# Kernel tuning notes

Hardware: AMD Instinct MI355X
Metric: run time of the kernel (lower is better)

Reference implementation:

```python
import jax, jax.numpy as jnp
import numpy as np

B, T, D, H = 2, 2048, 1024, 16
DK = D // H


def setup_inputs() -> dict:
    key = jax.random.key(0)
    ks = jax.random.split(key, 11)
    s = 1.0 / np.sqrt(D)
    return {
        "x_q": jax.random.normal(ks[0], (B, T, D), jnp.float32),
        "x_kv": jax.random.normal(ks[1], (B, T, D), jnp.float32),
        "mask": jnp.ones((B, 1, T, T), jnp.int32),
        "Wq": jax.random.normal(ks[2], (D, D), jnp.float32) * s,
        "bq": jnp.zeros((D,), jnp.float32),
        "Wk": jax.random.normal(ks[3], (D, D), jnp.float32) * s,
        "bk": jnp.zeros((D,), jnp.float32),
        "Wv": jax.random.normal(ks[4], (D, D), jnp.float32) * s,
        "bv": jnp.zeros((D,), jnp.float32),
        "Wo": jax.random.normal(ks[5], (D, D), jnp.float32) * s,
        "bo": jnp.zeros((D,), jnp.float32),
    }


def _split_heads(x):
    # (B, T, D) -> (B, H, T, DK)
    b, t, _ = x.shape
    return x.reshape(b, t, H, DK).transpose(0, 2, 1, 3)


def reference(x_q, x_kv, mask, Wq, bq, Wk, bk, Wv, bv, Wo, bo):
    # Linear layers use torch convention: y = x @ W.T + b
    Q = _split_heads(x_q @ Wq.T + bq)   # (B,H,Tq,DK)
    K = _split_heads(x_kv @ Wk.T + bk)  # (B,H,Tk,DK)
    V = _split_heads(x_kv @ Wv.T + bv)  # (B,H,Tk,DK)

    scores = jnp.einsum("bhqd,bhkd->bhqk", Q, K) / jnp.sqrt(jnp.float32(DK))
    scores = jnp.where(mask == 0, jnp.float32(-jnp.inf), scores)
    attn = jax.nn.softmax(scores, axis=-1)  # (B,H,Tq,Tk)

    out = jnp.einsum("bhqk,bhkd->bhqd", attn, V)
    out = out.transpose(0, 2, 1, 3).reshape(B, T, D)  # combine heads
    out = out @ Wo.T + bo
    return out, attn
```

## Files before the change

kernel.cpp:

```cpp
#include <hip/hip_runtime.h>
#include <hip/hip_bf16.h>

#define DEVINL __device__ __forceinline__

typedef __attribute__((ext_vector_type(4))) float f32x4;
typedef __attribute__((ext_vector_type(8))) short short8;

constexpr int CB = 2, CT = 2048, CD = 1024, CH = 16, CDK = 64;
constexpr int CM = CB * CT;
constexpr float LOG2E = 1.44269504088896340736f;

DEVINL ushort f2bf(float f) {
  __hip_bfloat16 h = __float2bfloat16(f);
  ushort u; __builtin_memcpy(&u, &h, 2); return u;
}

DEVINL void gl2lds16(const ushort* g, ushort* ldsbase) {
  __builtin_amdgcn_global_load_lds(
      (const __attribute__((address_space(1))) void*)g,
      (__attribute__((address_space(3))) void*)ldsbase, 16, 0, 0);
}

__global__ void cvt_all_kernel(const float* __restrict__ s0, ushort* __restrict__ d0, int n0,
                               const float* __restrict__ s1, ushort* __restrict__ d1, int n1,
                               const float* __restrict__ s2, ushort* __restrict__ d2, int n2,
                               const float* __restrict__ s3, ushort* __restrict__ d3, int n3,
                               const float* __restrict__ s4, ushort* __restrict__ d4, int n4,
                               const float* __restrict__ s5, ushort* __restrict__ d5, int n5)
{
  int i = (blockIdx.x * blockDim.x + threadIdx.x) * 4;
  const float* s; ushort* d;
  if (i < n0) { s = s0; d = d0; }
  else if ((i -= n0) < n1) { s = s1; d = d1; }
  else if ((i -= n1) < n2) { s = s2; d = d2; }
  else if ((i -= n2) < n3) { s = s3; d = d3; }
  else if ((i -= n3) < n4) { s = s4; d = d4; }
  else if ((i -= n4) < n5) { s = s5; d = d5; }
  else return;
  float4 v = *reinterpret_cast<const float4*>(s + i);
  ushort4 o;
  o.x = f2bf(v.x); o.y = f2bf(v.y); o.z = f2bf(v.z); o.w = f2bf(v.w);
  *reinterpret_cast<ushort4*>(d + i) = o;
}

__global__ void mask_flags_kernel(const int* __restrict__ mask, uint* __restrict__ flags) {
  const int tile = blockIdx.x;
  const int b = tile >> 10, qb = (tile >> 5) & 31, kb = tile & 31;
  const int* base = mask + ((size_t)b * CT + qb * 64) * CT + kb * 64;
  const int r = threadIdx.x >> 2, c0 = (threadIdx.x & 3) * 16;
  int ok = 1;
  for (int j = 0; j < 4; ++j) {
    int4 v = *reinterpret_cast<const int4*>(base + (size_t)r * CT + c0 + j * 4);
    ok &= (v.x != 0) & (v.y != 0) & (v.z != 0) & (v.w != 0);
  }
  __shared__ int red[4];
  unsigned long long bal = __ballot(ok);
  if ((threadIdx.x & 63) == 0) red[threadIdx.x >> 6] = (bal == ~0ull);
  __syncthreads();
  if (threadIdx.x == 0) flags[tile] = (uint)(red[0] & red[1] & red[2] & red[3]);
}

__global__ __launch_bounds__(256, 2)
void gemm_nt_kernel(const ushort* __restrict__ A, const ushort* __restrict__ Bm,
                    const float* __restrict__ bias1, const float* __restrict__ bias2,
                    void* __restrict__ Out, void* __restrict__ Out2,
                    int M, int N, int K, int mode, float scale)
{
  constexpr int BM = 128, BN = 64, BK = 32;
  __shared__ __align__(16) ushort As[2][BM * BK];
  __shared__ __align__(16) ushort Bs[2][BN * BK];
  const int tid = threadIdx.x;
  const int lane = tid & 63, wid = tid >> 6;
  const int wr = wid >> 1, wc = wid & 1;
  const int bm0 = blockIdx.y * BM, bn0 = blockIdx.x * BN;
  const int rsel = lane & 15, ksel = (lane >> 4) * 8;
  const int srow = lane >> 2, sc8 = (lane & 3) * 8;

  f32x4 acc[4][2];
  for (int i = 0; i < 4; ++i) for (int j = 0; j < 2; ++j) acc[i][j] = f32x4{0.f, 0.f, 0.f, 0.f};

  auto stage = [&](int bu, int k0) {
    const int ra0 = wid * 32;
    gl2lds16(&A[(size_t)(bm0 + ra0 + srow) * K + k0 + sc8],      &As[bu][ra0 * BK]);
    gl2lds16(&A[(size_t)(bm0 + ra0 + 16 + srow) * K + k0 + sc8], &As[bu][(ra0 + 16) * BK]);
    const int rb0 = wid * 16;
    gl2lds16(&Bm[(size_t)(bn0 + rb0 + srow) * K + k0 + sc8],     &Bs[bu][rb0 * BK]);
  };

  stage(0, 0);
  __syncthreads();
  const int NKT = K / BK;
  int bu = 0;
  for (int kt = 0; kt < NKT; ++kt) {
    if (kt + 1 < NKT) stage(bu ^ 1, (kt + 1) * BK);
    short8 af[4], bfr[2];
    for (int mi = 0; mi < 4; ++mi)
      af[mi] = *reinterpret_cast<short8*>(&As[bu][(wr * 64 + mi * 16 + rsel) * BK + ksel]);
    for (int ni = 0; ni < 2; ++ni)
      bfr[ni] = *reinterpret_cast<short8*>(&Bs[bu][(wc * 32 + ni * 16 + rsel) * BK + ksel]);
    for (int mi = 0; mi < 4; ++mi)
      for (int ni = 0; ni < 2; ++ni)
        acc[mi][ni] = __builtin_amdgcn_mfma_f32_16x16x32_bf16(af[mi], bfr[ni], acc[mi][ni], 0, 0, 0);
    if (kt + 1 < NKT) { __syncthreads(); bu ^= 1; }
  }

  const int r0 = (lane >> 4) * 4;
  for (int mi = 0; mi < 4; ++mi)
    for (int ni = 0; ni < 2; ++ni) {
      int gj = bn0 + wc * 32 + ni * 16 + rsel;
      float bv = (mode == 3 && gj >= 1024) ? bias2[gj - 1024] : bias1[gj];
      for (int r = 0; r < 4; ++r) {
        int gi = bm0 + wr * 64 + mi * 16 + r0 + r;
        float v = (acc[mi][ni][r] + bv) * scale;
        if (mode == 2) {
          reinterpret_cast<float*>(Out)[(size_t)gi * N + gj] = v;
        } else {
          int bb = gi >> 11, t = gi & (CT - 1);
          if (mode == 3 && gj >= 1024) {
            int gjv = gj - 1024;
            reinterpret_cast<ushort*>(Out2)[(((size_t)(bb * CH + (gjv >> 6)) * CDK + (gjv & 63)) * CT + t)] = f2bf(v);
          } else {
            reinterpret_cast<ushort*>(Out)[(((size_t)(bb * CH + (gj >> 6)) * CT + t) * CDK + (gj & 63))] = f2bf(v);
          }
        }
      }
    }
}

__global__ __launch_bounds__(512, 2)
void attn_kernel(const ushort* __restrict__ Qb, const ushort* __restrict__ Kb,
                 const ushort* __restrict__ Vt, const int* __restrict__ mask,
                 const uint* __restrict__ flags,
                 float* __restrict__ attn_out, ushort* __restrict__ oh)
{
  constexpr int KB = 64, LDK = 72;
  __shared__ __align__(16) ushort Ks[KB * LDK];
  __shared__ __align__(16) ushort Vs[CDK * LDK];
  __shared__ __align__(16) ushort Ps[8][16 * LDK];

  const int tid = threadIdx.x, wid = tid >> 6, lane = tid & 63;
  const int bh = blockIdx.y, b = bh >> 4, h = bh & 15;
  const int q0 = blockIdx.x * 128 + wid * 16;
  const int rsel = lane & 15, grp = lane >> 4, ksel = grp * 8;
  const int srow = tid >> 3, scol = (tid & 7) * 8;
  const uint* fl = flags + (b << 10) + ((q0 >> 6) << 5);

  short8 qa0, qa1;
  {
    const ushort* qrow = Qb + ((size_t)bh * CT + q0 + rsel) * CDK;
    qa0 = *reinterpret_cast<const short8*>(qrow + ksel);
    qa1 = *reinterpret_cast<const short8*>(qrow + 32 + ksel);
  }

  float l_part[4] = {0.f, 0.f, 0.f, 0.f};
  const int* mrow = mask + (size_t)b * CT * CT;

  for (int k0 = 0; k0 < CT; k0 += KB) {
    __syncthreads();
    *reinterpret_cast<short8*>(&Ks[srow * LDK + scol]) =
        *reinterpret_cast<const short8*>(&Kb[((size_t)bh * CT + k0 + srow) * CDK + scol]);
    __syncthreads();
    const uint f = fl[k0 >> 6];
    for (int ni = 0; ni < 4; ++ni) {
      f32x4 z = {0.f, 0.f, 0.f, 0.f};
      short8 kb0 = *reinterpret_cast<short8*>(&Ks[(ni * 16 + rsel) * LDK + ksel]);
      short8 kb1 = *reinterpret_cast<short8*>(&Ks[(ni * 16 + rsel) * LDK + 32 + ksel]);
      z = __builtin_amdgcn_mfma_f32_16x16x32_bf16(qa0, kb0, z, 0, 0, 0);
      z = __builtin_amdgcn_mfma_f32_16x16x32_bf16(qa1, kb1, z, 0, 0, 0);
      if (f) {
        for (int r = 0; r < 4; ++r) l_part[r] += exp2f(z[r]);
      } else {
        int kk = k0 + ni * 16 + rsel;
        for (int r = 0; r < 4; ++r) {
          int q = q0 + grp * 4 + r;
          l_part[r] += mrow[(size_t)q * CT + kk] ? exp2f(z[r]) : 0.f;
        }
      }
    }
  }
  for (int off = 1; off < 16; off <<= 1)
    for (int r = 0; r < 4; ++r) l_part[r] += __shfl_xor(l_part[r], off, 64);
  float inv_l[4];
  for (int r = 0; r < 4; ++r) inv_l[r] = 1.f / l_part[r];

  f32x4 oacc[4];
  for (int nd = 0; nd < 4; ++nd) oacc[nd] = f32x4{0.f, 0.f, 0.f, 0.f};
  float* arow = attn_out + (size_t)bh * CT * CT;
  ushort* pw = &Ps[wid][0];

  for (int k0 = 0; k0 < CT; k0 += KB) {
    __syncthreads();
    *reinterpret_cast<short8*>(&Ks[srow * LDK + scol]) =
        *reinterpret_cast<const short8*>(&Kb[((size_t)bh * CT + k0 + srow) * CDK + scol]);
    *reinterpret_cast<short8*>(&Vs[srow * LDK + scol]) =
        *reinterpret_cast<const short8*>(&Vt[((size_t)bh * CDK + srow) * CT + k0 + scol]);
    __syncthreads();
    const uint f = fl[k0 >> 6];
    for (int ni = 0; ni < 4; ++ni) {
      f32x4 z = {0.f, 0.f, 0.f, 0.f};
      short8 kb0 = *reinterpret_cast<short8*>(&Ks[(ni * 16 + rsel) * LDK + ksel]);
      short8 kb1 = *reinterpret_cast<short8*>(&Ks[(ni * 16 + rsel) * LDK + 32 + ksel]);
      z = __builtin_amdgcn_mfma_f32_16x16x32_bf16(qa0, kb0, z, 0, 0, 0);
      z = __builtin_amdgcn_mfma_f32_16x16x32_bf16(qa1, kb1, z, 0, 0, 0);
      int kk = k0 + ni * 16 + rsel;
      for (int r = 0; r < 4; ++r) {
        int q = q0 + grp * 4 + r;
        float p;
        if (f) p = exp2f(z[r]);
        else   p = mrow[(size_t)q * CT + kk] ? exp2f(z[r]) : 0.f;
        arow[(size_t)q * CT + kk] = p * inv_l[r];
        pw[(grp * 4 + r) * LDK + ni * 16 + rsel] = f2bf(p);
      }
    }
    short8 pa0 = *reinterpret_cast<short8*>(&pw[rsel * LDK + ksel]);
    short8 pa1 = *reinterpret_cast<short8*>(&pw[rsel * LDK + 32 + ksel]);
    for (int nd = 0; nd < 4; ++nd) {
      short8 vb0 = *reinterpret_cast<short8*>(&Vs[(nd * 16 + rsel) * LDK + ksel]);
      short8 vb1 = *reinterpret_cast<short8*>(&Vs[(nd * 16 + rsel) * LDK + 32 + ksel]);
      oacc[nd] = __builtin_amdgcn_mfma_f32_16x16x32_bf16(pa0, vb0, oacc[nd], 0, 0, 0);
      oacc[nd] = __builtin_amdgcn_mfma_f32_16x16x32_bf16(pa1, vb1, oacc[nd], 0, 0, 0);
    }
  }

  for (int nd = 0; nd < 4; ++nd)
    for (int r = 0; r < 4; ++r) {
      int q = q0 + grp * 4 + r, d = nd * 16 + rsel;
      oh[((size_t)b * CT + q) * CD + h * CDK + d] = f2bf(oacc[nd][r] * inv_l[r]);
    }
}

extern "C" void kernel_launch(void* const* d_in, const int* in_sizes, int n_in,
                              void* d_out, int out_size, void* d_ws, size_t ws_size,
                              hipStream_t stream)
{
  const float* x_q  = (const float*)d_in[0];
  const float* x_kv = (const float*)d_in[1];
  const int*   mask = (const int*)d_in[2];
  const float* Wq = (const float*)d_in[3];
  const float* bq = (const float*)d_in[4];
  const float* Wk = (const float*)d_in[5];
  const float* bk = (const float*)d_in[6];
  const float* Wv = (const float*)d_in[7];
  const float* bv = (const float*)d_in[8];
  const float* Wo = (const float*)d_in[9];
  const float* bo = (const float*)d_in[10];

  float* out  = (float*)d_out;
  float* attn = out + (size_t)CB * CT * CD;

  char* w = (char*)d_ws;
  auto alloc = [&](size_t bytes) { char* p = w; w += (bytes + 255) & ~(size_t)255; return p; };
  ushort* xq_bf  = (ushort*)alloc((size_t)CM * CD * 2);
  ushort* xkv_bf = (ushort*)alloc((size_t)CM * CD * 2);
  ushort* Wq_bf  = (ushort*)alloc((size_t)CD * CD * 2);
  ushort* Wk_bf  = (ushort*)alloc((size_t)CD * CD * 2);
  ushort* Wv_bf  = (ushort*)alloc((size_t)CD * CD * 2);
  ushort* Wo_bf  = (ushort*)alloc((size_t)CD * CD * 2);
  ushort* Q_bf   = (ushort*)alloc((size_t)CM * CD * 2);
  ushort* K_bf   = (ushort*)alloc((size_t)CM * CD * 2);
  ushort* Vt_bf  = (ushort*)alloc((size_t)CM * CD * 2);
  ushort* oh_bf  = (ushort*)alloc((size_t)CM * CD * 2);
  uint*   mflags = (uint*)alloc(2048 * sizeof(uint));

  {
    const int nx = CM * CD, nw = CD * CD;
    const int total_quads = (2 * nx + 4 * nw) / 4;
    const int blocks = (total_quads + 255) / 256;
    hipLaunchKernelGGL(cvt_all_kernel, dim3(blocks), dim3(256), 0, stream,
                       x_q, xq_bf, nx, x_kv, xkv_bf, nx,
                       Wq, Wq_bf, nw, Wk, Wk_bf, nw,
                       Wv, Wv_bf, nw, Wo, Wo_bf, nw);
  }

  hipLaunchKernelGGL(mask_flags_kernel, dim3(2048), dim3(256), 0, stream, mask, mflags);

  hipLaunchKernelGGL(gemm_nt_kernel, dim3(CD / 64, CM / 128), dim3(256), 0, stream,
                     xq_bf, Wq_bf, bq, bq, (void*)Q_bf, nullptr, CM, CD, CD, 0, 0.125f * LOG2E);
  hipLaunchKernelGGL(gemm_nt_kernel, dim3(2 * CD / 64, CM / 128), dim3(256), 0, stream,
                     xkv_bf, Wk_bf, bk, bv, (void*)K_bf, (void*)Vt_bf, CM, 2 * CD, CD, 3, 1.0f);

  hipLaunchKernelGGL(attn_kernel, dim3(CT / 128, CB * CH), dim3(512), 0, stream,
                     Q_bf, K_bf, Vt_bf, mask, mflags, attn, oh_bf);

  hipLaunchKernelGGL(gemm_nt_kernel, dim3(CD / 64, CM / 128), dim3(256), 0, stream,
                     oh_bf, Wo_bf, bo, bo, d_out, nullptr, CM, CD, CD, 2, 1.0f);
}
```

Baseline: 331.5 us.

## Double-buffer K/V via async global-to-LDS loads with swizzle and transposed QK MFMA

Replaces the synchronous K/V LDS staging with double-buffered global_load_lds copies into XOR-swizzled LDS tiles, so the next tile's load overlaps compute and one barrier per iteration is removed. The QK MFMA operands are swapped so each lane holds four consecutive keys for one query row, which allows float4 stores of the attention matrix and packed 4-wide stores of P into LDS. The row-sum reduction is reorganized to match, and inverse norms are shuffled back for the output layout. This adds more LDS and relies on the swizzle matching the async copy layout.

```diff
diff --git a/kernel.cpp b/kernel.cpp
--- a/kernel.cpp
+++ b/kernel.cpp
@@ -5,6 +5,7 @@
 
 typedef __attribute__((ext_vector_type(4))) float f32x4;
 typedef __attribute__((ext_vector_type(8))) short short8;
+typedef __attribute__((ext_vector_type(4))) short short4v;
 
 constexpr int CB = 2, CT = 2048, CD = 1024, CH = 16, CDK = 64;
 constexpr int CM = CB * CT;
@@ -133,17 +134,28 @@
                  const uint* __restrict__ flags,
                  float* __restrict__ attn_out, ushort* __restrict__ oh)
 {
-  constexpr int KB = 64, LDK = 72;
-  __shared__ __align__(16) ushort Ks[KB * LDK];
-  __shared__ __align__(16) ushort Vs[CDK * LDK];
-  __shared__ __align__(16) ushort Ps[8][16 * LDK];
+  constexpr int LDP = 72;
+  __shared__ __align__(16) ushort Ks[2][64 * 64];
+  __shared__ __align__(16) ushort Vs[2][64 * 64];
+  __shared__ __align__(16) ushort Ps[8][16 * LDP];
 
   const int tid = threadIdx.x, wid = tid >> 6, lane = tid & 63;
   const int bh = blockIdx.y, b = bh >> 4, h = bh & 15;
   const int q0 = blockIdx.x * 128 + wid * 16;
   const int rsel = lane & 15, grp = lane >> 4, ksel = grp * 8;
-  const int srow = tid >> 3, scol = (tid & 7) * 8;
+  const int swz = rsel & 7;
   const uint* fl = flags + (b << 10) + ((q0 >> 6) << 5);
+  const ushort* kpan = Kb + (size_t)bh * CT * CDK;
+  const ushort* vpan = Vt + (size_t)bh * CDK * CT;
+
+  const int strow = tid >> 3, stc = (tid & 7) ^ (strow & 7);
+
+  auto stageK = [&](int bu, int k0) {
+    gl2lds16(&kpan[(size_t)(k0 + strow) * CDK + stc * 8], &Ks[bu][(size_t)wid * 512]);
+  };
+  auto stageV = [&](int bu, int k0) {
+    gl2lds16(&vpan[(size_t)strow * CT + k0 + stc * 8], &Vs[bu][(size_t)wid * 512]);
+  };
 
   short8 qa0, qa1;
   {
@@ -152,80 +164,94 @@
     qa1 = *reinterpret_cast<const short8*>(qrow + 32 + ksel);
   }
 
-  float l_part[4] = {0.f, 0.f, 0.f, 0.f};
   const int* mrow = mask + (size_t)b * CT * CT;
-
-  for (int k0 = 0; k0 < CT; k0 += KB) {
+  const int qme = q0 + rsel;
+
+  float l_lane = 0.f;
+  stageK(0, 0);
+  __syncthreads();
+  int bu = 0;
+  for (int kt = 0; kt < 32; ++kt) {
+    const int k0 = kt * 64;
+    if (kt + 1 < 32) stageK(bu ^ 1, k0 + 64);
+    const uint f = fl[kt];
+    for (int ni = 0; ni < 4; ++ni) {
+      const int krow = ni * 16 + rsel;
+      short8 kb0 = *reinterpret_cast<short8*>(&Ks[bu][krow * 64 + ((grp    ) ^ swz) * 8]);
+      short8 kb1 = *reinterpret_cast<short8*>(&Ks[bu][krow * 64 + ((grp + 4) ^ swz) * 8]);
+      f32x4 z = {0.f, 0.f, 0.f, 0.f};
+      z = __builtin_amdgcn_mfma_f32_16x16x32_bf16(kb0, qa0, z, 0, 0, 0);
+      z = __builtin_amdgcn_mfma_f32_16x16x32_bf16(kb1, qa1, z, 0, 0, 0);
+      if (f) {
+        l_lane += exp2f(z[0]) + exp2f(z[1]) + exp2f(z[2]) + exp2f(z[3]);
+      } else {
+        const int kb_ = k0 + ni * 16 + grp * 4;
+        for (int r = 0; r < 4; ++r)
+          l_lane += mrow[(size_t)qme * CT + kb_ + r] ? exp2f(z[r]) : 0.f;
+      }
+    }
     __syncthreads();
-    *reinterpret_cast<short8*>(&Ks[srow * LDK + scol]) =
-        *reinterpret_cast<const short8*>(&Kb[((size_t)bh * CT + k0 + srow) * CDK + scol]);
-    __syncthreads();
-    const uint f = fl[k0 >> 6];
-    for (int ni = 0; ni < 4; ++ni) {
-      f32x4 z = {0.f, 0.f, 0.f, 0.f};
-      short8 kb0 = *reinterpret_cast<short8*>(&Ks[(ni * 16 + rsel) * LDK + ksel]);
-      short8 kb1 = *reinterpret_cast<short8*>(&Ks[(ni * 16 + rsel) * LDK + 32 + ksel]);
-      z = __builtin_amdgcn_mfma_f32_16x16x32_bf16(qa0, kb0, z, 0, 0, 0);
-      z = __builtin_amdgcn_mfma_f32_16x16x32_bf16(qa1, kb1, z, 0, 0, 0);
-      if (f) {
-        for (int r = 0; r < 4; ++r) l_part[r] += exp2f(z[r]);
-      } else {
-        int kk = k0 + ni * 16 + rsel;
-        for (int r = 0; r < 4; ++r) {
-          int q = q0 + grp * 4 + r;
-          l_part[r] += mrow[(size_t)q * CT + kk] ? exp2f(z[r]) : 0.f;
-        }
-      }
-    }
-  }
-  for (int off = 1; off < 16; off <<= 1)
-    for (int r = 0; r < 4; ++r) l_part[r] += __shfl_xor(l_part[r], off, 64);
-  float inv_l[4];
-  for (int r = 0; r < 4; ++r) inv_l[r] = 1.f / l_part[r];
+    bu ^= 1;
+  }
+  l_lane += __shfl_xor(l_lane, 16, 64);
+  l_lane += __shfl_xor(l_lane, 32, 64);
+  const float inv_l = 1.f / l_lane;
 
   f32x4 oacc[4];
   for (int nd = 0; nd < 4; ++nd) oacc[nd] = f32x4{0.f, 0.f, 0.f, 0.f};
-  float* arow = attn_out + (size_t)bh * CT * CT;
+  float* aq = attn_out + (size_t)bh * CT * CT + (size_t)qme * CT;
   ushort* pw = &Ps[wid][0];
 
-  for (int k0 = 0; k0 < CT; k0 += KB) {
-    __syncthreads();
-    *reinterpret_cast<short8*>(&Ks[srow * LDK + scol]) =
-        *reinterpret_cast<const short8*>(&Kb[((size_t)bh * CT + k0 + srow) * CDK + scol]);
-    *reinterpret_cast<short8*>(&Vs[srow * LDK + scol]) =
-        *reinterpret_cast<const short8*>(&Vt[((size_t)bh * CDK + srow) * CT + k0 + scol]);
-    __syncthreads();
-    const uint f = fl[k0 >> 6];
+  stageK(0, 0);
+  stageV(0, 0);
+  __syncthreads();
+  bu = 0;
+  for (int kt = 0; kt < 32; ++kt) {
+    const int k0 = kt * 64;
+    if (kt + 1 < 32) { stageK(bu ^ 1, k0 + 64); stageV(bu ^ 1, k0 + 64); }
+    const uint f = fl[kt];
     for (int ni = 0; ni < 4; ++ni) {
+      const int krow = ni * 16 + rsel;
+      short8 kb0 = *reinterpret_cast<short8*>(&Ks[bu][krow * 64 + ((grp    ) ^ swz) * 8]);
+      short8 kb1 = *reinterpret_cast<short8*>(&Ks[bu][krow * 64 + ((grp + 4) ^ swz) * 8]);
       f32x4 z = {0.f, 0.f, 0.f, 0.f};
-      short8 kb0 = *reinterpret_cast<short8*>(&Ks[(ni * 16 + rsel) * LDK + ksel]);
-      short8 kb1 = *reinterpret_cast<short8*>(&Ks[(ni * 16 + rsel) * LDK + 32 + ksel]);
-      z = __builtin_amdgcn_mfma_f32_16x16x32_bf16(qa0, kb0, z, 0, 0, 0);
-      z = __builtin_amdgcn_mfma_f32_16x16x32_bf16(qa1, kb1, z, 0, 0, 0);
-      int kk = k0 + ni * 16 + rsel;
-      for (int r = 0; r < 4; ++r) {
-        int q = q0 + grp * 4 + r;
-        float p;
-        if (f) p = exp2f(z[r]);
-        else   p = mrow[(size_t)q * CT + kk] ? exp2f(z[r]) : 0.f;
-        arow[(size_t)q * CT + kk] = p * inv_l[r];
-        pw[(grp * 4 + r) * LDK + ni * 16 + rsel] = f2bf(p);
+      z = __builtin_amdgcn_mfma_f32_16x16x32_bf16(kb0, qa0, z, 0, 0, 0);
+      z = __builtin_amdgcn_mfma_f32_16x16x32_bf16(kb1, qa1, z, 0, 0, 0);
+      const int kb_ = k0 + ni * 16 + grp * 4;
+      float p0, p1, p2, p3;
+      if (f) {
+        p0 = exp2f(z[0]); p1 = exp2f(z[1]); p2 = exp2f(z[2]); p3 = exp2f(z[3]);
+      } else {
+        const size_t mb = (size_t)qme * CT + kb_;
+        p0 = mrow[mb + 0] ? exp2f(z[0]) : 0.f;
+        p1 = mrow[mb + 1] ? exp2f(z[1]) : 0.f;
+        p2 = mrow[mb + 2] ? exp2f(z[2]) : 0.f;
+        p3 = mrow[mb + 3] ? exp2f(z[3]) : 0.f;
       }
-    }
-    short8 pa0 = *reinterpret_cast<short8*>(&pw[rsel * LDK + ksel]);
-    short8 pa1 = *reinterpret_cast<short8*>(&pw[rsel * LDK + 32 + ksel]);
+      float4 st = make_float4(p0 * inv_l, p1 * inv_l, p2 * inv_l, p3 * inv_l);
+      *reinterpret_cast<float4*>(aq + kb_) = st;
+      short4v pk = {(short)f2bf(p0), (short)f2bf(p1), (short)f2bf(p2), (short)f2bf(p3)};
+      *reinterpret_cast<short4v*>(&pw[rsel * LDP + ni * 16 + grp * 4]) = pk;
+    }
+    short8 pa0 = *reinterpret_cast<short8*>(&pw[rsel * LDP + ksel]);
+    short8 pa1 = *reinterpret_cast<short8*>(&pw[rsel * LDP + 32 + ksel]);
     for (int nd = 0; nd < 4; ++nd) {
-      short8 vb0 = *reinterpret_cast<short8*>(&Vs[(nd * 16 + rsel) * LDK + ksel]);
-      short8 vb1 = *reinterpret_cast<short8*>(&Vs[(nd * 16 + rsel) * LDK + 32 + ksel]);
+      const int vrow = nd * 16 + rsel;
+      short8 vb0 = *reinterpret_cast<short8*>(&Vs[bu][vrow * 64 + ((grp    ) ^ swz) * 8]);
+      short8 vb1 = *reinterpret_cast<short8*>(&Vs[bu][vrow * 64 + ((grp + 4) ^ swz) * 8]);
       oacc[nd] = __builtin_amdgcn_mfma_f32_16x16x32_bf16(pa0, vb0, oacc[nd], 0, 0, 0);
       oacc[nd] = __builtin_amdgcn_mfma_f32_16x16x32_bf16(pa1, vb1, oacc[nd], 0, 0, 0);
     }
-  }
-
+    __syncthreads();
+    bu ^= 1;
+  }
+
+  float invl_o[4];
+  for (int r = 0; r < 4; ++r) invl_o[r] = __shfl(inv_l, grp * 4 + r, 16);
   for (int nd = 0; nd < 4; ++nd)
     for (int r = 0; r < 4; ++r) {
       int q = q0 + grp * 4 + r, d = nd * 16 + rsel;
-      oh[((size_t)b * CT + q) * CD + h * CDK + d] = f2bf(oacc[nd][r] * inv_l[r]);
+      oh[((size_t)b * CT + q) * CD + h * CDK + d] = f2bf(oacc[nd][r] * invl_o[r]);
     }
 }
 
```

Result: no change. 330.7 us (-0.2%).
